# Performance work log

Measured on AMD Instinct MI355X. Metric: run time of the kernel, lower is better.

The kernel has to match this reference:

```python
import jax, jax.numpy as jnp
import numpy as np

SCALE = 1.0

def setup_inputs() -> dict:
    key = jax.random.key(0)
    ks = jax.random.split(key, 7)
    B, S, I, O, R = 4, 4096, 1024, 1024, 256
    return {
        "x": jax.random.normal(ks[0], (B, S, I), dtype=jnp.float32),
        "base_weight": jax.random.normal(ks[1], (3 * O, I), dtype=jnp.float32) * 0.02,
        "base_bias": jax.random.normal(ks[2], (3 * O,), dtype=jnp.float32) * 0.02,
        "vera_A": jax.random.normal(ks[3], (R, I), dtype=jnp.float32) * 0.02,
        "vera_B": jax.random.normal(ks[4], (O, R), dtype=jnp.float32) * 0.02,
        "vera_d": jax.random.normal(ks[5], (2, R), dtype=jnp.float32) * 0.1,
        "vera_b": jax.random.normal(ks[6], (2, O), dtype=jnp.float32) * 0.1,
    }

def reference(x, base_weight, base_bias, vera_A, vera_B, vera_d, vera_b):
    # delta[k] = scale * diag(vera_b[k]) @ B @ diag(vera_d[k]) @ A  for k in {K, V}
    # implemented as (b[:,None]*B) @ (d[:,None]*A), batched over k via einsum
    O, I = vera_B.shape[0], vera_A.shape[1]
    deltas = SCALE * jnp.einsum("ko,or,kr,ri->koi", vera_b, vera_B, vera_d, vera_A)
    delta = deltas.reshape(2 * O, I)  # (2*O, I) stacked K,V deltas
    # kv_only=True: Q rows get zero delta, then K,V deltas
    zeros = jnp.zeros((base_weight.shape[0] - 2 * O, I), dtype=base_weight.dtype)
    full_delta = jnp.concatenate([zeros, delta], axis=0)  # (3*O, I)
    weight = base_weight + full_delta
    # linear: x @ weight.T + bias -> (B, S, 3*O)
    return jnp.einsum("bsi,oi->bso", x, weight) + base_bias
```

## Files before the change

kernel.cpp:

```cpp
#include <hip/hip_runtime.h>
#include <hip/hip_bf16.h>
#include <cstdint>
#include <cstddef>

typedef __bf16 bf16_t;
typedef __bf16 bf16x8 __attribute__((ext_vector_type(8)));
typedef __bf16 bf16x4 __attribute__((ext_vector_type(4)));
typedef float  f32x4  __attribute__((ext_vector_type(4)));

#define M_DIM 16384
#define N_DIM 3072
#define K_DIM 1024
#define R_DIM 256
#define O_DIM 1024

#define BM 128
#define BN 128
#define BK 32

__global__ __launch_bounds__(256) void convert_x(
    const float* __restrict__ x, bf16_t* __restrict__ xh)
{
  const size_t base = ((size_t)blockIdx.x * 256 + threadIdx.x) * 8;
  const f32x4 v0 = *(const f32x4*)(x + base);
  const f32x4 v1 = *(const f32x4*)(x + base + 4);
  bf16x8 o;
  o[0] = (bf16_t)v0[0]; o[1] = (bf16_t)v0[1]; o[2] = (bf16_t)v0[2]; o[3] = (bf16_t)v0[3];
  o[4] = (bf16_t)v1[0]; o[5] = (bf16_t)v1[1]; o[6] = (bf16_t)v1[2]; o[7] = (bf16_t)v1[3];
  *(bf16x8*)(xh + base) = o;
}

__global__ __launch_bounds__(256) void prep_weight(
    const float* __restrict__ base_w,
    const float* __restrict__ vA,
    const float* __restrict__ vB,
    const float* __restrict__ vd,
    const float* __restrict__ vb,
    bf16_t* __restrict__ Wf)
{
  const int blk = blockIdx.x;
  const int t = threadIdx.x;

  if (blk < 128) {
    const float* src = base_w + (size_t)blk * 8 * K_DIM;
    bf16_t*      dst = Wf + (size_t)blk * 8 * K_DIM;
#pragma unroll
    for (int rr = 0; rr < 8; ++rr) {
      const f32x4 v = *(const f32x4*)(src + rr * K_DIM + t * 4);
      bf16x4 ov;
      ov[0] = (bf16_t)v[0]; ov[1] = (bf16_t)v[1];
      ov[2] = (bf16_t)v[2]; ov[3] = (bf16_t)v[3];
      *(bf16x4*)(dst + rr * K_DIM + t * 4) = ov;
    }
    return;
  }

  const int rb = (blk - 128) * 8;
  const int k  = rb >> 10;
  const int ob = rb & 1023;

  __shared__ float coeffT[R_DIM][8];
  {
    const int r = t;
    const float d = vd[k * R_DIM + r];
#pragma unroll
    for (int rr = 0; rr < 8; ++rr) {
      const int o = ob + rr;
      coeffT[r][rr] = vb[k * O_DIM + o] * vB[(size_t)o * R_DIM + r] * d;
    }
  }
  __syncthreads();

  float acc[8][4];
#pragma unroll
  for (int rr = 0; rr < 8; ++rr)
#pragma unroll
    for (int c = 0; c < 4; ++c) acc[rr][c] = 0.0f;

  for (int r = 0; r < R_DIM; ++r) {
    const f32x4 av = *(const f32x4*)(vA + (size_t)r * K_DIM + t * 4);
    const f32x4 c0 = *(const f32x4*)&coeffT[r][0];
    const f32x4 c1 = *(const f32x4*)&coeffT[r][4];
#pragma unroll
    for (int rr = 0; rr < 8; ++rr) {
      const float cc = (rr < 4) ? c0[rr] : c1[rr - 4];
      acc[rr][0] += cc * av[0];
      acc[rr][1] += cc * av[1];
      acc[rr][2] += cc * av[2];
      acc[rr][3] += cc * av[3];
    }
  }

#pragma unroll
  for (int rr = 0; rr < 8; ++rr) {
    const size_t row = (size_t)(1024 + rb + rr);
    const f32x4 bw = *(const f32x4*)(base_w + row * K_DIM + t * 4);
    bf16x4 ov;
    ov[0] = (bf16_t)(bw[0] + acc[rr][0]);
    ov[1] = (bf16_t)(bw[1] + acc[rr][1]);
    ov[2] = (bf16_t)(bw[2] + acc[rr][2]);
    ov[3] = (bf16_t)(bw[3] + acc[rr][3]);
    *(bf16x4*)(Wf + row * K_DIM + t * 4) = ov;
  }
}

template <bool PRECONV>
__global__ __launch_bounds__(256) void gemm_qkv(
    const bf16_t* __restrict__ Xh,
    const float*  __restrict__ Xf,
    const bf16_t* __restrict__ W,
    const float*  __restrict__ bias,
    float* __restrict__ out)
{
  __shared__ bf16_t As[BM * BK];
  __shared__ bf16_t Bs[BN * BK];

  const int bid = blockIdx.x;
  const int nt = bid % (N_DIM / BN);
  const int mt = bid / (N_DIM / BN);
  const int m0 = mt * BM;
  const int n0 = nt * BN;

  const int t = threadIdx.x;
  const int lane = t & 63;
  const int w = t >> 6;
  const int wm = w >> 1;
  const int wn = w & 1;

  const int sr = t >> 2;
  const int sc = (t & 3) * 8;

  const bf16_t* gB0 = W + (size_t)(n0 + sr) * K_DIM + sc;
  const bf16_t* gB1 = gB0 + (size_t)64 * K_DIM;

  bf16x8 ra0, ra1;
  uint4 rb0, rb1;

  const bf16_t* gA0h = Xh + (size_t)(m0 + sr) * K_DIM + sc;
  const bf16_t* gA1h = gA0h + (size_t)64 * K_DIM;
  const float*  gA0f = Xf + (size_t)(m0 + sr) * K_DIM + sc;
  const float*  gA1f = gA0f + (size_t)64 * K_DIM;

  if (PRECONV) {
    ra0 = *(const bf16x8*)(gA0h);
    ra1 = *(const bf16x8*)(gA1h);
  } else {
    const f32x4 u0 = *(const f32x4*)(gA0f), u1 = *(const f32x4*)(gA0f + 4);
    const f32x4 u2 = *(const f32x4*)(gA1f), u3 = *(const f32x4*)(gA1f + 4);
#pragma unroll
    for (int c = 0; c < 4; ++c) { ra0[c] = (bf16_t)u0[c]; ra0[c + 4] = (bf16_t)u1[c]; }
#pragma unroll
    for (int c = 0; c < 4; ++c) { ra1[c] = (bf16_t)u2[c]; ra1[c + 4] = (bf16_t)u3[c]; }
  }
  rb0 = *(const uint4*)(gB0);
  rb1 = *(const uint4*)(gB1);

  const f32x4 zero4 = {0.0f, 0.0f, 0.0f, 0.0f};
  f32x4 acc[4][4];
#pragma unroll
  for (int i = 0; i < 4; ++i)
#pragma unroll
    for (int j = 0; j < 4; ++j) acc[i][j] = zero4;

  const int row_a = wm * 64 + (lane & 15);
  const int row_b = wn * 64 + (lane & 15);
  const int kb = (lane >> 4) * 8;

  for (int k0 = 0; k0 < K_DIM; k0 += BK) {
    *(bf16x8*)(As + sr * BK + sc)        = ra0;
    *(bf16x8*)(As + (sr + 64) * BK + sc) = ra1;
    *(uint4*)(Bs + sr * BK + sc)         = rb0;
    *(uint4*)(Bs + (sr + 64) * BK + sc)  = rb1;
    __syncthreads();

    if (k0 + BK < K_DIM) {
      if (PRECONV) {
        ra0 = *(const bf16x8*)(gA0h + k0 + BK);
        ra1 = *(const bf16x8*)(gA1h + k0 + BK);
      } else {
        const f32x4 u0 = *(const f32x4*)(gA0f + k0 + BK);
        const f32x4 u1 = *(const f32x4*)(gA0f + k0 + BK + 4);
        const f32x4 u2 = *(const f32x4*)(gA1f + k0 + BK);
        const f32x4 u3 = *(const f32x4*)(gA1f + k0 + BK + 4);
#pragma unroll
        for (int c = 0; c < 4; ++c) { ra0[c] = (bf16_t)u0[c]; ra0[c + 4] = (bf16_t)u1[c]; }
#pragma unroll
        for (int c = 0; c < 4; ++c) { ra1[c] = (bf16_t)u2[c]; ra1[c + 4] = (bf16_t)u3[c]; }
      }
      rb0 = *(const uint4*)(gB0 + k0 + BK);
      rb1 = *(const uint4*)(gB1 + k0 + BK);
    }

    bf16x8 a[4], b[4];
#pragma unroll
    for (int i = 0; i < 4; ++i)
      a[i] = *(const bf16x8*)(As + (row_a + i * 16) * BK + kb);
#pragma unroll
    for (int j = 0; j < 4; ++j)
      b[j] = *(const bf16x8*)(Bs + (row_b + j * 16) * BK + kb);

#pragma unroll
    for (int i = 0; i < 4; ++i)
#pragma unroll
      for (int j = 0; j < 4; ++j)
        acc[i][j] = __builtin_amdgcn_mfma_f32_16x16x32_bf16(a[i], b[j], acc[i][j], 0, 0, 0);

    __syncthreads();
  }

  const int colg = lane & 15;
  const int rq = (lane >> 4) * 4;
#pragma unroll
  for (int j = 0; j < 4; ++j) {
    const int n = n0 + wn * 64 + j * 16 + colg;
    const float bv = bias[n];
#pragma unroll
    for (int i = 0; i < 4; ++i) {
      const size_t mb = (size_t)(m0 + wm * 64 + i * 16 + rq);
#pragma unroll
      for (int r = 0; r < 4; ++r)
        out[(mb + r) * N_DIM + n] = acc[i][j][r] + bv;
    }
  }
}

extern "C" void kernel_launch(void* const* d_in, const int* in_sizes, int n_in,
                              void* d_out, int out_size, void* d_ws, size_t ws_size,
                              hipStream_t stream) {
  const float* x      = (const float*)d_in[0];
  const float* base_w = (const float*)d_in[1];
  const float* base_b = (const float*)d_in[2];
  const float* vA     = (const float*)d_in[3];
  const float* vB     = (const float*)d_in[4];
  const float* vd     = (const float*)d_in[5];
  const float* vb     = (const float*)d_in[6];
  float* out = (float*)d_out;

  const size_t wf_bytes = (size_t)N_DIM * K_DIM * sizeof(bf16_t);
  const size_t xh_off   = 8u * 1024 * 1024;
  const size_t xh_bytes = (size_t)M_DIM * K_DIM * sizeof(bf16_t);

  bf16_t* Wf = (bf16_t*)d_ws;
  prep_weight<<<384, 256, 0, stream>>>(base_w, vA, vB, vd, vb, Wf);

  const int gemm_grid = (M_DIM / BM) * (N_DIM / BN);
  if (ws_size >= xh_off + xh_bytes) {
    bf16_t* Xh = (bf16_t*)((char*)d_ws + xh_off);
    convert_x<<<(M_DIM * K_DIM) / (256 * 8), 256, 0, stream>>>(x, Xh);
    gemm_qkv<true><<<gemm_grid, 256, 0, stream>>>(Xh, nullptr, Wf, base_b, out);
  } else {
    gemm_qkv<false><<<gemm_grid, 256, 0, stream>>>(nullptr, x, Wf, base_b, out);
  }
}
```

Before: 424.3 us.

## Merge prep kernels, use direct global-to-LDS loads and XCD-aware tile swizzle

Fuses the x conversion and weight preparation into a single launch, which removes one kernel launch. The GEMM now loads tiles with global_load_lds, writing straight into shared memory instead of staging them in registers. This also drops the register prefetch, so loads are no longer overlapped with the MFMA work of the previous iteration. Block IDs are remapped so each XCD handles a contiguous range of tiles, aiming for better L2 reuse. The risk is that global load latency is now exposed each iteration, because there is no double buffering.

```diff
diff --git a/kernel.cpp b/kernel.cpp
--- a/kernel.cpp
+++ b/kernel.cpp
@@ -17,29 +17,39 @@
 #define BM 128
 #define BN 128
 #define BK 32
-
-__global__ __launch_bounds__(256) void convert_x(
-    const float* __restrict__ x, bf16_t* __restrict__ xh)
-{
-  const size_t base = ((size_t)blockIdx.x * 256 + threadIdx.x) * 8;
-  const f32x4 v0 = *(const f32x4*)(x + base);
-  const f32x4 v1 = *(const f32x4*)(x + base + 4);
-  bf16x8 o;
-  o[0] = (bf16_t)v0[0]; o[1] = (bf16_t)v0[1]; o[2] = (bf16_t)v0[2]; o[3] = (bf16_t)v0[3];
-  o[4] = (bf16_t)v1[0]; o[5] = (bf16_t)v1[1]; o[6] = (bf16_t)v1[2]; o[7] = (bf16_t)v1[3];
-  *(bf16x8*)(xh + base) = o;
-}
-
-__global__ __launch_bounds__(256) void prep_weight(
+#define NT_TILES 24
+#define GRID_GEMM 3072
+#define CHUNK_XCD 384
+
+__device__ __forceinline__ void gload_lds16(const bf16_t* g, bf16_t* l) {
+  __builtin_amdgcn_global_load_lds(
+      (__attribute__((address_space(1))) void*)(g),
+      (__attribute__((address_space(3))) void*)(l), 16, 0, 0);
+}
+
+__global__ __launch_bounds__(256) void prep_all(
+    const float* __restrict__ x,
     const float* __restrict__ base_w,
     const float* __restrict__ vA,
     const float* __restrict__ vB,
     const float* __restrict__ vd,
     const float* __restrict__ vb,
-    bf16_t* __restrict__ Wf)
+    bf16_t* __restrict__ Wf,
+    bf16_t* __restrict__ xh)
 {
   const int blk = blockIdx.x;
   const int t = threadIdx.x;
+
+  if (blk >= 384) {
+    const size_t base = ((size_t)(blk - 384) * 256 + t) * 8;
+    const f32x4 v0 = *(const f32x4*)(x + base);
+    const f32x4 v1 = *(const f32x4*)(x + base + 4);
+    bf16x8 o;
+    o[0] = (bf16_t)v0[0]; o[1] = (bf16_t)v0[1]; o[2] = (bf16_t)v0[2]; o[3] = (bf16_t)v0[3];
+    o[4] = (bf16_t)v1[0]; o[5] = (bf16_t)v1[1]; o[6] = (bf16_t)v1[2]; o[7] = (bf16_t)v1[3];
+    *(bf16x8*)(xh + base) = o;
+    return;
+  }
 
   if (blk < 128) {
     const float* src = base_w + (size_t)blk * 8 * K_DIM;
@@ -115,9 +125,10 @@
   __shared__ bf16_t As[BM * BK];
   __shared__ bf16_t Bs[BN * BK];
 
-  const int bid = blockIdx.x;
-  const int nt = bid % (N_DIM / BN);
-  const int mt = bid / (N_DIM / BN);
+  const int rawbid = blockIdx.x;
+  const int bid = (rawbid & 7) * CHUNK_XCD + (rawbid >> 3);
+  const int nt = bid % NT_TILES;
+  const int mt = bid / NT_TILES;
   const int m0 = mt * BM;
   const int n0 = nt * BN;
 
@@ -127,33 +138,25 @@
   const int wm = w >> 1;
   const int wn = w & 1;
 
-  const int sr = t >> 2;
-  const int sc = (t & 3) * 8;
-
-  const bf16_t* gB0 = W + (size_t)(n0 + sr) * K_DIM + sc;
+  const int r0 = t >> 2;
+  const int c0 = (t & 3) * 8;
+
+  const bf16_t* gB0 = W + (size_t)(n0 + r0) * K_DIM + c0;
   const bf16_t* gB1 = gB0 + (size_t)64 * K_DIM;
-
-  bf16x8 ra0, ra1;
-  uint4 rb0, rb1;
-
-  const bf16_t* gA0h = Xh + (size_t)(m0 + sr) * K_DIM + sc;
-  const bf16_t* gA1h = gA0h + (size_t)64 * K_DIM;
-  const float*  gA0f = Xf + (size_t)(m0 + sr) * K_DIM + sc;
-  const float*  gA1f = gA0f + (size_t)64 * K_DIM;
-
-  if (PRECONV) {
-    ra0 = *(const bf16x8*)(gA0h);
-    ra1 = *(const bf16x8*)(gA1h);
+  bf16_t* lA0 = As + r0 * BK + c0;
+  bf16_t* lA1 = As + (r0 + 64) * BK + c0;
+  bf16_t* lB0 = Bs + r0 * BK + c0;
+  bf16_t* lB1 = Bs + (r0 + 64) * BK + c0;
+
+  const bf16_t* gA0h = nullptr; const bf16_t* gA1h = nullptr;
+  const float*  gA0f = nullptr; const float*  gA1f = nullptr;
+  if constexpr (PRECONV) {
+    gA0h = Xh + (size_t)(m0 + r0) * K_DIM + c0;
+    gA1h = gA0h + (size_t)64 * K_DIM;
   } else {
-    const f32x4 u0 = *(const f32x4*)(gA0f), u1 = *(const f32x4*)(gA0f + 4);
-    const f32x4 u2 = *(const f32x4*)(gA1f), u3 = *(const f32x4*)(gA1f + 4);
-#pragma unroll
-    for (int c = 0; c < 4; ++c) { ra0[c] = (bf16_t)u0[c]; ra0[c + 4] = (bf16_t)u1[c]; }
-#pragma unroll
-    for (int c = 0; c < 4; ++c) { ra1[c] = (bf16_t)u2[c]; ra1[c + 4] = (bf16_t)u3[c]; }
-  }
-  rb0 = *(const uint4*)(gB0);
-  rb1 = *(const uint4*)(gB1);
+    gA0f = Xf + (size_t)(m0 + r0) * K_DIM + c0;
+    gA1f = gA0f + (size_t)64 * K_DIM;
+  }
 
   const f32x4 zero4 = {0.0f, 0.0f, 0.0f, 0.0f};
   f32x4 acc[4][4];
@@ -167,29 +170,26 @@
   const int kb = (lane >> 4) * 8;
 
   for (int k0 = 0; k0 < K_DIM; k0 += BK) {
-    *(bf16x8*)(As + sr * BK + sc)        = ra0;
-    *(bf16x8*)(As + (sr + 64) * BK + sc) = ra1;
-    *(uint4*)(Bs + sr * BK + sc)         = rb0;
-    *(uint4*)(Bs + (sr + 64) * BK + sc)  = rb1;
+    if constexpr (PRECONV) {
+      gload_lds16(gA0h + k0, lA0);
+      gload_lds16(gA1h + k0, lA1);
+    } else {
+      const f32x4 u0 = *(const f32x4*)(gA0f + k0);
+      const f32x4 u1 = *(const f32x4*)(gA0f + k0 + 4);
+      const f32x4 u2 = *(const f32x4*)(gA1f + k0);
+      const f32x4 u3 = *(const f32x4*)(gA1f + k0 + 4);
+      bf16x8 a0, a1;
+#pragma unroll
+      for (int c = 0; c < 4; ++c) {
+        a0[c] = (bf16_t)u0[c]; a0[c + 4] = (bf16_t)u1[c];
+        a1[c] = (bf16_t)u2[c]; a1[c + 4] = (bf16_t)u3[c];
+      }
+      *(bf16x8*)lA0 = a0;
+      *(bf16x8*)lA1 = a1;
+    }
+    gload_lds16(gB0 + k0, lB0);
+    gload_lds16(gB1 + k0, lB1);
     __syncthreads();
-
-    if (k0 + BK < K_DIM) {
-      if (PRECONV) {
-        ra0 = *(const bf16x8*)(gA0h + k0 + BK);
-        ra1 = *(const bf16x8*)(gA1h + k0 + BK);
-      } else {
-        const f32x4 u0 = *(const f32x4*)(gA0f + k0 + BK);
-        const f32x4 u1 = *(const f32x4*)(gA0f + k0 + BK + 4);
-        const f32x4 u2 = *(const f32x4*)(gA1f + k0 + BK);
-        const f32x4 u3 = *(const f32x4*)(gA1f + k0 + BK + 4);
-#pragma unroll
-        for (int c = 0; c < 4; ++c) { ra0[c] = (bf16_t)u0[c]; ra0[c + 4] = (bf16_t)u1[c]; }
-#pragma unroll
-        for (int c = 0; c < 4; ++c) { ra1[c] = (bf16_t)u2[c]; ra1[c + 4] = (bf16_t)u3[c]; }
-      }
-      rb0 = *(const uint4*)(gB0 + k0 + BK);
-      rb1 = *(const uint4*)(gB1 + k0 + BK);
-    }
 
     bf16x8 a[4], b[4];
 #pragma unroll
@@ -236,19 +236,17 @@
   const float* vb     = (const float*)d_in[6];
   float* out = (float*)d_out;
 
-  const size_t wf_bytes = (size_t)N_DIM * K_DIM * sizeof(bf16_t);
   const size_t xh_off   = 8u * 1024 * 1024;
   const size_t xh_bytes = (size_t)M_DIM * K_DIM * sizeof(bf16_t);
 
   bf16_t* Wf = (bf16_t*)d_ws;
-  prep_weight<<<384, 256, 0, stream>>>(base_w, vA, vB, vd, vb, Wf);
-
-  const int gemm_grid = (M_DIM / BM) * (N_DIM / BN);
-  if (ws_size >= xh_off + xh_bytes) {
-    bf16_t* Xh = (bf16_t*)((char*)d_ws + xh_off);
-    convert_x<<<(M_DIM * K_DIM) / (256 * 8), 256, 0, stream>>>(x, Xh);
-    gemm_qkv<true><<<gemm_grid, 256, 0, stream>>>(Xh, nullptr, Wf, base_b, out);
-  } else {
-    gemm_qkv<false><<<gemm_grid, 256, 0, stream>>>(nullptr, x, Wf, base_b, out);
-  }
-}
+  const bool preconv = ws_size >= xh_off + xh_bytes;
+  bf16_t* Xh = preconv ? (bf16_t*)((char*)d_ws + xh_off) : nullptr;
+
+  prep_all<<<preconv ? 8576 : 384, 256, 0, stream>>>(x, base_w, vA, vB, vd, vb, Wf, Xh);
+
+  if (preconv)
+    gemm_qkv<true><<<GRID_GEMM, 256, 0, stream>>>(Xh, nullptr, Wf, base_b, out);
+  else
+    gemm_qkv<false><<<GRID_GEMM, 256, 0, stream>>>(nullptr, x, Wf, base_b, out);
+}
```

Result: no change. 422.0 us (-0.5%).
